# Performance work log

Hardware: AMD Instinct MI355X
Metric: run time of the kernel (lower is better)

Reference implementation:

```python
import jax, jax.numpy as jnp
import numpy as np

K = 1024   # number of NNLS components (theta_1 is K x K)
B = 8192   # batched frames / columns


def setup_inputs() -> dict:
    key = jax.random.key(0)
    k1, k2, k3, k4 = jax.random.split(key, 4)
    # theta_1 = I - AtA / ||AtA||_F  -> near-identity contraction; emulate with
    # identity minus a small random symmetric-ish perturbation.
    pert = jax.random.normal(k1, (K, K), dtype=jnp.float32) * (1.0 / K)
    th1 = jnp.eye(K, dtype=jnp.float32) - pert
    Y = jax.random.uniform(k2, (K, B), dtype=jnp.float32)
    X_old = jax.random.uniform(k3, (K, B), dtype=jnp.float32)
    weight = jax.random.normal(k4, (K, B), dtype=jnp.float32) * 0.1  # theta_2 = Atb/n_AtA
    k = 2  # PGD iteration counter
    return {"th1": th1, "Y": Y, "X_old": X_old, "k": k, "weight": weight}


def reference(th1, Y, X_old, k, weight):
    # One projected-gradient-descent step of NNLS with Nesterov momentum:
    #   new_X = relu(th1 @ Y + weight)
    #   Y_new = new_X + (k-1)/(k+2) * (new_X - X_old)
    kf = jnp.float32(k)
    new_X = jax.nn.relu(jnp.matmul(th1, Y) + weight)          # [K, B]
    momentum = (kf - 1.0) / (kf + 2.0)
    Y_new = new_X + momentum * (new_X - X_old)                # [K, B]
    return (Y_new, new_X, k + 1, weight)
```

## Files before the change

kernel.cpp:

```cpp
#include <hip/hip_runtime.h>
#include <cstdint>


#define KDIM 1024
#define NDIM 8192
#define KB_ELEMS (1024UL * 8192UL)
#define YT_BYTES (8192UL * 1024UL * 2UL)
#define AB_BYTES (1024UL * 1024UL * 2UL)
#define WS_NEED (YT_BYTES + AB_BYTES)

typedef short short8 __attribute__((ext_vector_type(8)));
typedef float f32x4 __attribute__((ext_vector_type(4)));

struct __attribute__((aligned(4))) f4u { float x, y, z, w; };

__device__ __forceinline__ uint32_t pk2(float a, float b) {
  uint32_t ua = __builtin_bit_cast(uint32_t, a) + 0x8000u;
  uint32_t ub = __builtin_bit_cast(uint32_t, b) + 0x8000u;
  return (ua >> 16) | (ub & 0xFFFF0000u);
}

__device__ __forceinline__ void ldsload16(const void* g, void* l) {
  __builtin_amdgcn_global_load_lds(
      (const __attribute__((address_space(1))) uint32_t*)g,
      (__attribute__((address_space(3))) uint32_t*)l, 16, 0, 0);
}

__global__ __launch_bounds__(256) void nnls_conv(
    const float* __restrict__ th1, const float* __restrict__ Y,
    char* __restrict__ ws)
{
  unsigned short* yt  = (unsigned short*)ws;
  unsigned short* abf = (unsigned short*)(ws + YT_BYTES);
  const int tid = threadIdx.x;
  if (blockIdx.x < 1024) {
    const int kt = blockIdx.x >> 5;
    const int n  = (blockIdx.x & 31) * 256 + tid;
    const float* src = Y + (size_t)kt * 32 * NDIM + n;
    float v[32];
#pragma unroll
    for (int r = 0; r < 32; ++r) v[r] = src[(size_t)r * NDIM];
    __attribute__((aligned(16))) uint32_t o[16];
#pragma unroll
    for (int r = 0; r < 16; ++r) o[r] = pk2(v[2 * r], v[2 * r + 1]);
    const int perm = (n >> 1) & 3;
    uint4* dst = (uint4*)(yt + ((size_t)kt * NDIM + n) * 32);
    const uint4* o4 = (const uint4*)o;
#pragma unroll
    for (int q = 0; q < 4; ++q) dst[q ^ perm] = o4[q];
  } else {
    const int id = (blockIdx.x - 1024) * 256 + tid;
    const int kt = id >> 10, m = id & 1023;
    const float4* s4 = (const float4*)(th1 + (size_t)m * KDIM + kt * 32);
    __attribute__((aligned(16))) uint32_t o[16];
#pragma unroll
    for (int q = 0; q < 8; ++q) {
      const float4 v = s4[q];
      o[2 * q]     = pk2(v.x, v.y);
      o[2 * q + 1] = pk2(v.z, v.w);
    }
    const int perm = (m >> 1) & 3;
    uint4* dst = (uint4*)(abf + ((size_t)kt * KDIM + m) * 32);
    const uint4* o4 = (const uint4*)o;
#pragma unroll
    for (int q = 0; q < 4; ++q) dst[q ^ perm] = o4[q];
  }
}

__global__ __launch_bounds__(256, 4) void nnls_gemm5(
    const char* __restrict__ ws, const float* __restrict__ xold,
    const int* __restrict__ kin, const float* __restrict__ weight,
    float* __restrict__ out)
{
  const char* yt = ws;
  const char* ab = ws + YT_BYTES;
  __shared__ __align__(16) char smem[36864];

  const int tid  = threadIdx.x;
  const int lane = tid & 63;
  const int w    = tid >> 6;
  const int wm = w >> 1, wn = w & 1;
  const int quad = lane >> 4, nl = lane & 15;

  const int m0 = blockIdx.y * 128;
  const int n0 = blockIdx.x * 64;

  const char* ag = ab + (size_t)m0 * 64 + w * 1024 + lane * 16;
  const char* bg = yt + (size_t)n0 * 64 + w * 1024 + lane * 16;

  auto stage = [&](int kt, int buf) {
    const char* a2 = ag + (size_t)kt * 65536;
    const char* b2 = bg + (size_t)kt * 524288;
    char* d = smem + buf * 12288;
    ldsload16(a2,        d + w * 1024);
    ldsload16(a2 + 4096, d + 4096 + w * 1024);
    ldsload16(b2,        d + 8192 + w * 1024);
  };

  stage(0, 0);
  stage(1, 1);

  f32x4 acc[4][2] = {};
  const int fro = (quad ^ ((nl >> 1) & 3)) * 8;

#pragma unroll
  for (int kt = 0; kt < 32; ++kt) {
    if (kt == 31) { asm volatile("s_waitcnt vmcnt(0)" ::: "memory"); }
    else          { asm volatile("s_waitcnt vmcnt(3)" ::: "memory"); }
    __builtin_amdgcn_s_barrier();
    if (kt < 30) stage(kt + 2, (kt + 2) % 3);

    const unsigned short* Asp = (const unsigned short*)(smem + (kt % 3) * 12288);
    const unsigned short* Bsp = Asp + 4096;
    short8 af[4], bf[2];
#pragma unroll
    for (int i = 0; i < 4; ++i)
      af[i] = *(const short8*)&Asp[(wm * 64 + i * 16 + nl) * 32 + fro];
#pragma unroll
    for (int j = 0; j < 2; ++j)
      bf[j] = *(const short8*)&Bsp[(wn * 32 + j * 16 + nl) * 32 + fro];
#pragma unroll
    for (int i = 0; i < 4; ++i)
#pragma unroll
      for (int j = 0; j < 2; ++j)
        acc[i][j] = __builtin_amdgcn_mfma_f32_16x16x32_bf16(af[i], bf[j], acc[i][j], 0, 0, 0);
  }

  const float kf  = (float)kin[0];
  const float mom = (kf - 1.0f) / (kf + 2.0f);
  float* ep = (float*)smem + w * 576;
  const int rl = lane >> 3;
  const int cc = lane & 7;

#pragma unroll
  for (int i = 0; i < 4; ++i) {
    const int mgb = m0 + wm * 64 + i * 16;
    size_t idxs[2]; float4 wv[2], xo[2];
#pragma unroll
    for (int t = 0; t < 2; ++t) {
      idxs[t] = (size_t)(mgb + t * 8 + rl) * NDIM + n0 + wn * 32 + cc * 4;
      wv[t] = *(const float4*)&weight[idxs[t]];
      xo[t] = *(const float4*)&xold[idxs[t]];
    }
#pragma unroll
    for (int j = 0; j < 2; ++j)
#pragma unroll
      for (int r = 0; r < 4; ++r)
        ep[(quad * 4 + r) * 36 + j * 16 + nl] = acc[i][j][r];
#pragma unroll
    for (int t = 0; t < 2; ++t) {
      const float4 cv = *(const float4*)&ep[(t * 8 + rl) * 36 + cc * 4];
      const size_t idx = idxs[t];
      float4 nx, yn;
      nx.x = fmaxf(cv.x + wv[t].x, 0.0f); nx.y = fmaxf(cv.y + wv[t].y, 0.0f);
      nx.z = fmaxf(cv.z + wv[t].z, 0.0f); nx.w = fmaxf(cv.w + wv[t].w, 0.0f);
      yn.x = nx.x + mom * (nx.x - xo[t].x); yn.y = nx.y + mom * (nx.y - xo[t].y);
      yn.z = nx.z + mom * (nx.z - xo[t].z); yn.w = nx.w + mom * (nx.w - xo[t].w);
      *(float4*)&out[idx] = yn;
      *(float4*)&out[KB_ELEMS + idx] = nx;
      f4u s; s.x = wv[t].x; s.y = wv[t].y; s.z = wv[t].z; s.w = wv[t].w;
      *(f4u*)&out[2 * KB_ELEMS + 1 + idx] = s;
    }
  }

  if (blockIdx.x == 0 && blockIdx.y == 0 && tid == 0)
    out[2 * KB_ELEMS] = (float)(kin[0] + 1);
}

#define LDA 40
__global__ __launch_bounds__(512, 4) void nnls_gemm_v1(
    const float* __restrict__ th1, const float* __restrict__ Y,
    const float* __restrict__ xold, const int* __restrict__ kin,
    const float* __restrict__ weight, float* __restrict__ out)
{
  __shared__ __align__(16) char smem[40960];
  unsigned short* As0 = (unsigned short*)smem;
  unsigned short* Bs0 = (unsigned short*)(smem + 10240);
  unsigned short* As1 = (unsigned short*)(smem + 20480);
  unsigned short* Bs1 = (unsigned short*)(smem + 30720);

  const int tid  = threadIdx.x;
  const int lane = tid & 63;
  const int w    = tid >> 6;
  const int wm = w >> 1, wn = w & 1;
  const int quad = lane >> 4, nl = lane & 15;
  const int m0 = blockIdx.y * 128;
  const int n0 = blockIdx.x * 128;
  const int ar = tid >> 3;
  const int ac = tid & 7;
  const float* abase = th1 + (size_t)(m0 + ar) * KDIM + ac * 4;
  const int bn = tid & 127;
  const int bk = (tid >> 7) * 8;
  const float* ybase = Y + (size_t)bk * NDIM + n0 + bn;

  float4 abv[2];
  float  yb[8];
  abv[0] = *(const float4*)(abase);
  abv[1] = *(const float4*)(abase + (size_t)64 * KDIM);
#pragma unroll
  for (int r = 0; r < 8; ++r) yb[r] = ybase[(size_t)r * NDIM];

  f32x4 acc[2][4] = {};

#pragma unroll 2
  for (int kt = 0; kt < 32; ++kt) {
    unsigned short* Asp = (kt & 1) ? As1 : As0;
    unsigned short* Bsp = (kt & 1) ? Bs1 : Bs0;
    {
      uint2 d0; d0.x = pk2(abv[0].x, abv[0].y); d0.y = pk2(abv[0].z, abv[0].w);
      *(uint2*)&Asp[ar * LDA + ac * 4] = d0;
      uint2 d1; d1.x = pk2(abv[1].x, abv[1].y); d1.y = pk2(abv[1].z, abv[1].w);
      *(uint2*)&Asp[(ar + 64) * LDA + ac * 4] = d1;
      uint4 e;
      e.x = pk2(yb[0], yb[1]); e.y = pk2(yb[2], yb[3]);
      e.z = pk2(yb[4], yb[5]); e.w = pk2(yb[6], yb[7]);
      *(uint4*)&Bsp[bn * LDA + bk] = e;
    }
    __syncthreads();
    if (kt < 31) {
      const float* an = abase + (kt + 1) * 32;
      abv[0] = *(const float4*)(an);
      abv[1] = *(const float4*)(an + (size_t)64 * KDIM);
      const float* yn = ybase + (size_t)((kt + 1) * 32) * NDIM;
#pragma unroll
      for (int r = 0; r < 8; ++r) yb[r] = yn[(size_t)r * NDIM];
    }
    short8 af[2], bf[4];
#pragma unroll
    for (int i = 0; i < 2; ++i)
      af[i] = *(const short8*)&Asp[(wm * 32 + i * 16 + nl) * LDA + quad * 8];
#pragma unroll
    for (int j = 0; j < 4; ++j)
      bf[j] = *(const short8*)&Bsp[(wn * 64 + j * 16 + nl) * LDA + quad * 8];
#pragma unroll
    for (int i = 0; i < 2; ++i)
#pragma unroll
      for (int j = 0; j < 4; ++j)
        acc[i][j] = __builtin_amdgcn_mfma_f32_16x16x32_bf16(af[i], bf[j], acc[i][j], 0, 0, 0);
    __syncthreads();
  }
  __syncthreads();

  const float kf  = (float)kin[0];
  const float mom = (kf - 1.0f) / (kf + 2.0f);
  float* ep = (float*)smem + w * 1088;
  const int u  = lane >> 4;
  const int mc = lane & 15;
#pragma unroll
  for (int i = 0; i < 2; ++i) {
#pragma unroll
    for (int j = 0; j < 4; ++j)
#pragma unroll
      for (int r = 0; r < 4; ++r)
        ep[(quad * 4 + r) * 68 + (j * 16 + nl)] = acc[i][j][r];
    const int mgb = m0 + wm * 32 + i * 16;
#pragma unroll
    for (int t = 0; t < 4; ++t) {
      const int row = t * 4 + u;
      const float4 cv = *(const float4*)&ep[row * 68 + mc * 4];
      const int ng = n0 + wn * 64 + mc * 4;
      const size_t idx = (size_t)(mgb + row) * NDIM + ng;
      const float4 wv = *(const float4*)&weight[idx];
      const float4 xo = *(const float4*)&xold[idx];
      float4 nx, yn;
      nx.x = fmaxf(cv.x + wv.x, 0.0f); nx.y = fmaxf(cv.y + wv.y, 0.0f);
      nx.z = fmaxf(cv.z + wv.z, 0.0f); nx.w = fmaxf(cv.w + wv.w, 0.0f);
      yn.x = nx.x + mom * (nx.x - xo.x); yn.y = nx.y + mom * (nx.y - xo.y);
      yn.z = nx.z + mom * (nx.z - xo.z); yn.w = nx.w + mom * (nx.w - xo.w);
      *(float4*)&out[idx] = yn;
      *(float4*)&out[KB_ELEMS + idx] = nx;
      f4u s; s.x = wv.x; s.y = wv.y; s.z = wv.z; s.w = wv.w;
      *(f4u*)&out[2 * KB_ELEMS + 1 + idx] = s;
    }
  }
  if (blockIdx.x == 0 && blockIdx.y == 0 && tid == 0)
    out[2 * KB_ELEMS] = (float)(kin[0] + 1);
}

extern "C" void kernel_launch(void* const* d_in, const int* in_sizes, int n_in,
                              void* d_out, int out_size, void* d_ws, size_t ws_size,
                              hipStream_t stream) {
  const float* th1  = (const float*)d_in[0];
  const float* Y    = (const float*)d_in[1];
  const float* xold = (const float*)d_in[2];
  const int*   kin  = (const int*)d_in[3];
  const float* wgt  = (const float*)d_in[4];
  float* out = (float*)d_out;

  if (d_ws != nullptr && ws_size >= WS_NEED) {
    nnls_conv<<<1152, 256, 0, stream>>>(th1, Y, (char*)d_ws);
    nnls_gemm5<<<dim3(NDIM / 64, KDIM / 128), 256, 0, stream>>>(
        (const char*)d_ws, xold, kin, wgt, out);
  } else {
    nnls_gemm_v1<<<dim3(NDIM / 128, KDIM / 128), 512, 0, stream>>>(
        th1, Y, xold, kin, wgt, out);
  }
}
```

Before: 225.7 us.

## Enlarge GEMM tile to 256x128 with 512 threads and 32x32 MFMA

The block tile doubles in both dimensions (256x128) and uses 8 waves of 512 threads, each computing a 64x64 subtile. Fragments now use 32x32x16 bf16 MFMA instead of 16x16x32, and the epilogue is reworked to match the new accumulator layout. The aim is more operand reuse per LDS byte and fewer global loads per FLOP. The cost is fewer blocks (256 versus 1024), lower occupancy and a larger LDS footprint.

```diff
diff --git a/kernel.cpp b/kernel.cpp
--- a/kernel.cpp
+++ b/kernel.cpp
@@ -11,6 +11,7 @@
 
 typedef short short8 __attribute__((ext_vector_type(8)));
 typedef float f32x4 __attribute__((ext_vector_type(4)));
+typedef float f32x16 __attribute__((ext_vector_type(16)));
 
 struct __attribute__((aligned(4))) f4u { float x, y, z, w; };
 
@@ -67,23 +68,23 @@
   }
 }
 
-__global__ __launch_bounds__(256, 4) void nnls_gemm5(
+__global__ __launch_bounds__(512, 2) void nnls_gemm6(
     const char* __restrict__ ws, const float* __restrict__ xold,
     const int* __restrict__ kin, const float* __restrict__ weight,
     float* __restrict__ out)
 {
   const char* yt = ws;
   const char* ab = ws + YT_BYTES;
-  __shared__ __align__(16) char smem[36864];
+  __shared__ __align__(16) char smem[73728];
 
   const int tid  = threadIdx.x;
   const int lane = tid & 63;
   const int w    = tid >> 6;
   const int wm = w >> 1, wn = w & 1;
-  const int quad = lane >> 4, nl = lane & 15;
-
-  const int m0 = blockIdx.y * 128;
-  const int n0 = blockIdx.x * 64;
+  const int l5 = lane >> 5, l31 = lane & 31;
+
+  const int m0 = blockIdx.y * 256;
+  const int n0 = blockIdx.x * 128;
 
   const char* ag = ab + (size_t)m0 * 64 + w * 1024 + lane * 16;
   const char* bg = yt + (size_t)n0 * 64 + w * 1024 + lane * 16;
@@ -91,17 +92,16 @@
   auto stage = [&](int kt, int buf) {
     const char* a2 = ag + (size_t)kt * 65536;
     const char* b2 = bg + (size_t)kt * 524288;
-    char* d = smem + buf * 12288;
-    ldsload16(a2,        d + w * 1024);
-    ldsload16(a2 + 4096, d + 4096 + w * 1024);
-    ldsload16(b2,        d + 8192 + w * 1024);
+    char* d = smem + buf * 24576 + w * 1024;
+    ldsload16(a2,        d);
+    ldsload16(a2 + 8192, d + 8192);
+    ldsload16(b2,        d + 16384);
   };
 
   stage(0, 0);
   stage(1, 1);
 
-  f32x4 acc[4][2] = {};
-  const int fro = (quad ^ ((nl >> 1) & 3)) * 8;
+  f32x16 acc[2][2] = {};
 
 #pragma unroll
   for (int kt = 0; kt < 32; ++kt) {
@@ -110,58 +110,71 @@
     __builtin_amdgcn_s_barrier();
     if (kt < 30) stage(kt + 2, (kt + 2) % 3);
 
-    const unsigned short* Asp = (const unsigned short*)(smem + (kt % 3) * 12288);
-    const unsigned short* Bsp = Asp + 4096;
-    short8 af[4], bf[2];
-#pragma unroll
-    for (int i = 0; i < 4; ++i)
-      af[i] = *(const short8*)&Asp[(wm * 64 + i * 16 + nl) * 32 + fro];
-#pragma unroll
-    for (int j = 0; j < 2; ++j)
-      bf[j] = *(const short8*)&Bsp[(wn * 32 + j * 16 + nl) * 32 + fro];
-#pragma unroll
-    for (int i = 0; i < 4; ++i)
-#pragma unroll
-      for (int j = 0; j < 2; ++j)
-        acc[i][j] = __builtin_amdgcn_mfma_f32_16x16x32_bf16(af[i], bf[j], acc[i][j], 0, 0, 0);
-  }
+    const unsigned short* Asp = (const unsigned short*)(smem + (kt % 3) * 24576);
+    const unsigned short* Bsp = Asp + 8192;
+    short8 af[2][2], bf[2][2];
+#pragma unroll
+    for (int mi = 0; mi < 2; ++mi)
+#pragma unroll
+      for (int h = 0; h < 2; ++h) {
+        const int row = wm * 64 + mi * 32 + l31;
+        af[mi][h] = *(const short8*)&Asp[row * 32 + ((h * 2 + l5) ^ ((row >> 1) & 3)) * 8];
+      }
+#pragma unroll
+    for (int ni = 0; ni < 2; ++ni)
+#pragma unroll
+      for (int h = 0; h < 2; ++h) {
+        const int row = wn * 64 + ni * 32 + l31;
+        bf[ni][h] = *(const short8*)&Bsp[row * 32 + ((h * 2 + l5) ^ ((row >> 1) & 3)) * 8];
+      }
+#pragma unroll
+    for (int mi = 0; mi < 2; ++mi)
+#pragma unroll
+      for (int ni = 0; ni < 2; ++ni) {
+        acc[mi][ni] = __builtin_amdgcn_mfma_f32_32x32x16_bf16(af[mi][0], bf[ni][0], acc[mi][ni], 0, 0, 0);
+        acc[mi][ni] = __builtin_amdgcn_mfma_f32_32x32x16_bf16(af[mi][1], bf[ni][1], acc[mi][ni], 0, 0, 0);
+      }
+  }
+
+  __syncthreads();
 
   const float kf  = (float)kin[0];
   const float mom = (kf - 1.0f) / (kf + 2.0f);
-  float* ep = (float*)smem + w * 576;
+  float* ep = (float*)smem + w * 1152;
   const int rl = lane >> 3;
   const int cc = lane & 7;
 
 #pragma unroll
-  for (int i = 0; i < 4; ++i) {
-    const int mgb = m0 + wm * 64 + i * 16;
-    size_t idxs[2]; float4 wv[2], xo[2];
-#pragma unroll
-    for (int t = 0; t < 2; ++t) {
-      idxs[t] = (size_t)(mgb + t * 8 + rl) * NDIM + n0 + wn * 32 + cc * 4;
-      wv[t] = *(const float4*)&weight[idxs[t]];
-      xo[t] = *(const float4*)&xold[idxs[t]];
-    }
-#pragma unroll
-    for (int j = 0; j < 2; ++j)
-#pragma unroll
-      for (int r = 0; r < 4; ++r)
-        ep[(quad * 4 + r) * 36 + j * 16 + nl] = acc[i][j][r];
-#pragma unroll
-    for (int t = 0; t < 2; ++t) {
-      const float4 cv = *(const float4*)&ep[(t * 8 + rl) * 36 + cc * 4];
-      const size_t idx = idxs[t];
-      float4 nx, yn;
-      nx.x = fmaxf(cv.x + wv[t].x, 0.0f); nx.y = fmaxf(cv.y + wv[t].y, 0.0f);
-      nx.z = fmaxf(cv.z + wv[t].z, 0.0f); nx.w = fmaxf(cv.w + wv[t].w, 0.0f);
-      yn.x = nx.x + mom * (nx.x - xo[t].x); yn.y = nx.y + mom * (nx.y - xo[t].y);
-      yn.z = nx.z + mom * (nx.z - xo[t].z); yn.w = nx.w + mom * (nx.w - xo[t].w);
-      *(float4*)&out[idx] = yn;
-      *(float4*)&out[KB_ELEMS + idx] = nx;
-      f4u s; s.x = wv[t].x; s.y = wv[t].y; s.z = wv[t].z; s.w = wv[t].w;
-      *(f4u*)&out[2 * KB_ELEMS + 1 + idx] = s;
-    }
-  }
+  for (int mi = 0; mi < 2; ++mi)
+#pragma unroll
+    for (int ni = 0; ni < 2; ++ni) {
+      size_t idxs[4]; float4 wv[4], xo[4];
+#pragma unroll
+      for (int t = 0; t < 4; ++t) {
+        const int mg = m0 + wm * 64 + mi * 32 + t * 8 + rl;
+        const int ng = n0 + wn * 64 + ni * 32 + cc * 4;
+        idxs[t] = (size_t)mg * NDIM + ng;
+        wv[t] = *(const float4*)&weight[idxs[t]];
+        xo[t] = *(const float4*)&xold[idxs[t]];
+      }
+#pragma unroll
+      for (int g = 0; g < 16; ++g)
+        ep[((g & 3) + 8 * (g >> 2) + 4 * l5) * 36 + l31] = acc[mi][ni][g];
+#pragma unroll
+      for (int t = 0; t < 4; ++t) {
+        const float4 cv = *(const float4*)&ep[(t * 8 + rl) * 36 + cc * 4];
+        const size_t idx = idxs[t];
+        float4 nx, yn;
+        nx.x = fmaxf(cv.x + wv[t].x, 0.0f); nx.y = fmaxf(cv.y + wv[t].y, 0.0f);
+        nx.z = fmaxf(cv.z + wv[t].z, 0.0f); nx.w = fmaxf(cv.w + wv[t].w, 0.0f);
+        yn.x = nx.x + mom * (nx.x - xo[t].x); yn.y = nx.y + mom * (nx.y - xo[t].y);
+        yn.z = nx.z + mom * (nx.z - xo[t].z); yn.w = nx.w + mom * (nx.w - xo[t].w);
+        *(float4*)&out[idx] = yn;
+        *(float4*)&out[KB_ELEMS + idx] = nx;
+        f4u s; s.x = wv[t].x; s.y = wv[t].y; s.z = wv[t].z; s.w = wv[t].w;
+        *(f4u*)&out[2 * KB_ELEMS + 1 + idx] = s;
+      }
+    }
 
   if (blockIdx.x == 0 && blockIdx.y == 0 && tid == 0)
     out[2 * KB_ELEMS] = (float)(kin[0] + 1);
@@ -289,7 +302,7 @@
 
   if (d_ws != nullptr && ws_size >= WS_NEED) {
     nnls_conv<<<1152, 256, 0, stream>>>(th1, Y, (char*)d_ws);
-    nnls_gemm5<<<dim3(NDIM / 64, KDIM / 128), 256, 0, stream>>>(
+    nnls_gemm6<<<dim3(NDIM / 128, KDIM / 256), 512, 0, stream>>>(
         (const char*)d_ws, xold, kin, wgt, out);
   } else {
     nnls_gemm_v1<<<dim3(NDIM / 128, KDIM / 128), 512, 0, stream>>>(
```

New measurement: 238.8 us. 1.06x slower.

## Process two N-tiles per block and overlap first epilogue with second GEMM

Applied to the files above, without the earlier changes.

Each block now computes two adjacent 64-column output tiles in sequence over 64 k-steps, with a dedicated LDS region for the epilogue. The first tile's epilogue (weight/xold loads, relu, momentum, stores) is interleaved into the second tile's main loop so global memory traffic overlaps MFMA work. The grid is halved and the block index is remapped so that 8 consecutive blocks share the same B columns across all M tiles, improving L2 reuse. Costs are more registers (two accumulator sets), launch bounds lowered to 2 blocks per CU, and larger LDS use, which reduces occupancy.

```diff
diff --git a/kernel.cpp b/kernel.cpp
--- a/kernel.cpp
+++ b/kernel.cpp
@@ -67,14 +67,14 @@
   }
 }
 
-__global__ __launch_bounds__(256, 4) void nnls_gemm5(
+__global__ __launch_bounds__(256, 2) void nnls_gemm7(
     const char* __restrict__ ws, const float* __restrict__ xold,
     const int* __restrict__ kin, const float* __restrict__ weight,
     float* __restrict__ out)
 {
   const char* yt = ws;
   const char* ab = ws + YT_BYTES;
-  __shared__ __align__(16) char smem[36864];
+  __shared__ __align__(16) char smem[46080];
 
   const int tid  = threadIdx.x;
   const int lane = tid & 63;
@@ -82,33 +82,80 @@
   const int wm = w >> 1, wn = w & 1;
   const int quad = lane >> 4, nl = lane & 15;
 
-  const int m0 = blockIdx.y * 128;
-  const int n0 = blockIdx.x * 64;
+  const int f  = blockIdx.y * 64 + blockIdx.x;
+  const int m0 = (f & 7) * 128;
+  const int nx = f >> 3;
+  const int n0a = nx * 128, n0b = nx * 128 + 64;
 
   const char* ag = ab + (size_t)m0 * 64 + w * 1024 + lane * 16;
-  const char* bg = yt + (size_t)n0 * 64 + w * 1024 + lane * 16;
-
-  auto stage = [&](int kt, int buf) {
-    const char* a2 = ag + (size_t)kt * 65536;
-    const char* b2 = bg + (size_t)kt * 524288;
-    char* d = smem + buf * 12288;
+  const char* bg = yt + (size_t)(nx * 128) * 64 + w * 1024 + lane * 16;
+
+  auto stage = [&](int kt2) {
+    const char* a2 = ag + (size_t)(kt2 & 31) * 65536;
+    const char* b2 = bg + (size_t)(kt2 & 31) * 524288 + (kt2 >> 5) * 4096;
+    char* d = smem + (kt2 % 3) * 12288;
     ldsload16(a2,        d + w * 1024);
     ldsload16(a2 + 4096, d + 4096 + w * 1024);
     ldsload16(b2,        d + 8192 + w * 1024);
   };
 
-  stage(0, 0);
-  stage(1, 1);
-
-  f32x4 acc[4][2] = {};
+  stage(0);
+  stage(1);
+
+  f32x4 accA[4][2] = {}, accB[4][2] = {};
   const int fro = (quad ^ ((nl >> 1) & 3)) * 8;
 
-#pragma unroll
-  for (int kt = 0; kt < 32; ++kt) {
-    if (kt == 31) { asm volatile("s_waitcnt vmcnt(0)" ::: "memory"); }
-    else          { asm volatile("s_waitcnt vmcnt(3)" ::: "memory"); }
+  const float kf  = (float)kin[0];
+  const float mom = (kf - 1.0f) / (kf + 2.0f);
+  float* ep = (float*)(smem + 36864) + w * 576;
+  const int rl = lane >> 3;
+  const int cc = lane & 7;
+
+#define EPI_CHUNK(i, ACC, N0T)                                                  \
+  {                                                                             \
+    const int mgb = m0 + wm * 64 + (i) * 16;                                    \
+    size_t idxs[2]; float4 wv[2], xo[2];                                        \
+    _Pragma("unroll")                                                           \
+    for (int t = 0; t < 2; ++t) {                                               \
+      idxs[t] = (size_t)(mgb + t * 8 + rl) * NDIM + (N0T) + wn * 32 + cc * 4;   \
+      wv[t] = *(const float4*)&weight[idxs[t]];                                 \
+      xo[t] = *(const float4*)&xold[idxs[t]];                                   \
+    }                                                                           \
+    _Pragma("unroll")                                                           \
+    for (int j = 0; j < 2; ++j)                                                 \
+      _Pragma("unroll")                                                         \
+      for (int r = 0; r < 4; ++r)                                               \
+        ep[(quad * 4 + r) * 36 + j * 16 + nl] = ACC[i][j][r];                   \
+    _Pragma("unroll")                                                           \
+    for (int t = 0; t < 2; ++t) {                                               \
+      const float4 cv = *(const float4*)&ep[(t * 8 + rl) * 36 + cc * 4];        \
+      const size_t idx = idxs[t];                                               \
+      float4 nx_, yn;                                                           \
+      nx_.x = fmaxf(cv.x + wv[t].x, 0.0f); nx_.y = fmaxf(cv.y + wv[t].y, 0.0f); \
+      nx_.z = fmaxf(cv.z + wv[t].z, 0.0f); nx_.w = fmaxf(cv.w + wv[t].w, 0.0f); \
+      yn.x = nx_.x + mom * (nx_.x - xo[t].x); yn.y = nx_.y + mom * (nx_.y - xo[t].y); \
+      yn.z = nx_.z + mom * (nx_.z - xo[t].z); yn.w = nx_.w + mom * (nx_.w - xo[t].w); \
+      *(float4*)&out[idx] = yn;                                                 \
+      *(float4*)&out[KB_ELEMS + idx] = nx_;                                     \
+      f4u s_; s_.x = wv[t].x; s_.y = wv[t].y; s_.z = wv[t].z; s_.w = wv[t].w;   \
+      *(f4u*)&out[2 * KB_ELEMS + 1 + idx] = s_;                                 \
+    }                                                                           \
+  }
+
+#pragma unroll
+  for (int kt = 0; kt < 64; ++kt) {
+    if (kt == 63)      { asm volatile("s_waitcnt vmcnt(0)"  ::: "memory"); }
+    else if (kt == 35 || kt == 41 || kt == 47 || kt == 53)
+                       { asm volatile("s_waitcnt vmcnt(13)" ::: "memory"); }
+    else               { asm volatile("s_waitcnt vmcnt(3)"  ::: "memory"); }
     __builtin_amdgcn_s_barrier();
-    if (kt < 30) stage(kt + 2, (kt + 2) % 3);
+
+    if (kt == 34)      EPI_CHUNK(0, accA, n0a)
+    else if (kt == 40) EPI_CHUNK(1, accA, n0a)
+    else if (kt == 46) EPI_CHUNK(2, accA, n0a)
+    else if (kt == 52) EPI_CHUNK(3, accA, n0a)
+
+    if (kt < 62) stage(kt + 2);
 
     const unsigned short* Asp = (const unsigned short*)(smem + (kt % 3) * 12288);
     const unsigned short* Bsp = Asp + 4096;
@@ -119,51 +166,28 @@
 #pragma unroll
     for (int j = 0; j < 2; ++j)
       bf[j] = *(const short8*)&Bsp[(wn * 32 + j * 16 + nl) * 32 + fro];
-#pragma unroll
-    for (int i = 0; i < 4; ++i)
-#pragma unroll
-      for (int j = 0; j < 2; ++j)
-        acc[i][j] = __builtin_amdgcn_mfma_f32_16x16x32_bf16(af[i], bf[j], acc[i][j], 0, 0, 0);
-  }
-
-  const float kf  = (float)kin[0];
-  const float mom = (kf - 1.0f) / (kf + 2.0f);
-  float* ep = (float*)smem + w * 576;
-  const int rl = lane >> 3;
-  const int cc = lane & 7;
-
-#pragma unroll
-  for (int i = 0; i < 4; ++i) {
-    const int mgb = m0 + wm * 64 + i * 16;
-    size_t idxs[2]; float4 wv[2], xo[2];
-#pragma unroll
-    for (int t = 0; t < 2; ++t) {
-      idxs[t] = (size_t)(mgb + t * 8 + rl) * NDIM + n0 + wn * 32 + cc * 4;
-      wv[t] = *(const float4*)&weight[idxs[t]];
-      xo[t] = *(const float4*)&xold[idxs[t]];
-    }
-#pragma unroll
-    for (int j = 0; j < 2; ++j)
-#pragma unroll
-      for (int r = 0; r < 4; ++r)
-        ep[(quad * 4 + r) * 36 + j * 16 + nl] = acc[i][j][r];
-#pragma unroll
-    for (int t = 0; t < 2; ++t) {
-      const float4 cv = *(const float4*)&ep[(t * 8 + rl) * 36 + cc * 4];
-      const size_t idx = idxs[t];
-      float4 nx, yn;
-      nx.x = fmaxf(cv.x + wv[t].x, 0.0f); nx.y = fmaxf(cv.y + wv[t].y, 0.0f);
-      nx.z = fmaxf(cv.z + wv[t].z, 0.0f); nx.w = fmaxf(cv.w + wv[t].w, 0.0f);
-      yn.x = nx.x + mom * (nx.x - xo[t].x); yn.y = nx.y + mom * (nx.y - xo[t].y);
-      yn.z = nx.z + mom * (nx.z - xo[t].z); yn.w = nx.w + mom * (nx.w - xo[t].w);
-      *(float4*)&out[idx] = yn;
-      *(float4*)&out[KB_ELEMS + idx] = nx;
-      f4u s; s.x = wv[t].x; s.y = wv[t].y; s.z = wv[t].z; s.w = wv[t].w;
-      *(f4u*)&out[2 * KB_ELEMS + 1 + idx] = s;
-    }
-  }
-
-  if (blockIdx.x == 0 && blockIdx.y == 0 && tid == 0)
+    if (kt < 32) {
+#pragma unroll
+      for (int i = 0; i < 4; ++i)
+#pragma unroll
+        for (int j = 0; j < 2; ++j)
+          accA[i][j] = __builtin_amdgcn_mfma_f32_16x16x32_bf16(af[i], bf[j], accA[i][j], 0, 0, 0);
+    } else {
+#pragma unroll
+      for (int i = 0; i < 4; ++i)
+#pragma unroll
+        for (int j = 0; j < 2; ++j)
+          accB[i][j] = __builtin_amdgcn_mfma_f32_16x16x32_bf16(af[i], bf[j], accB[i][j], 0, 0, 0);
+    }
+  }
+
+  EPI_CHUNK(0, accB, n0b)
+  EPI_CHUNK(1, accB, n0b)
+  EPI_CHUNK(2, accB, n0b)
+  EPI_CHUNK(3, accB, n0b)
+#undef EPI_CHUNK
+
+  if (f == 0 && tid == 0)
     out[2 * KB_ELEMS] = (float)(kin[0] + 1);
 }
 
@@ -289,7 +313,7 @@
 
   if (d_ws != nullptr && ws_size >= WS_NEED) {
     nnls_conv<<<1152, 256, 0, stream>>>(th1, Y, (char*)d_ws);
-    nnls_gemm5<<<dim3(NDIM / 64, KDIM / 128), 256, 0, stream>>>(
+    nnls_gemm7<<<dim3(64, 8), 256, 0, stream>>>(
         (const char*)d_ws, xold, kin, wgt, out);
   } else {
     nnls_gemm_v1<<<dim3(NDIM / 128, KDIM / 128), 512, 0, stream>>>(
```

Result: slower. 275.7 us (+22.2%).
